# Optimization experiments

Hardware: AMD Instinct MI355X
Metric: run time of the kernel (lower is better)

The kernel has to match this reference:

```python
import jax, jax.numpy as jnp
import numpy as np

B, T, D, H, MLP, NI, OUT = 256, 2049, 64, 64, 128, 128, 10
L = D + D * (D - 1) // 2  # depth-2 logsignature channels = 2080


def _logsig_depth2(X, n_intervals):
    """Depth-2 log-signature of a piecewise-linear path over equal intervals.
    X: [B, T, D] with T = n_intervals*s + 1. Returns [B, n_intervals, L] where
    L = D + D(D-1)/2 (level-1 increments + strictly-upper-triangular Levy areas,
    the Lyndon-word basis signatory uses at depth 2)."""
    Bq, Tq, Dq = X.shape
    s = (Tq - 1) // n_intervals
    idx = np.arange(n_intervals)[:, None] * s + np.arange(s + 1)[None, :]
    seg = X[:, idx]                       # [B, n, s+1, D]
    inc = seg[:, :, -1] - seg[:, :, 0]    # level 1: [B, n, D]
    dlt = seg[:, :, 1:] - seg[:, :, :-1]  # per-step increments [B, n, s, D]
    cum = seg[:, :, :-1] - seg[:, :, :1]  # partial increments  [B, n, s, D]
    M = jnp.einsum('bnki,bnkj->bnij', cum, dlt)
    A = 0.5 * (M - jnp.swapaxes(M, -1, -2))  # Levy area [B, n, D, D]
    iu, ju = np.triu_indices(Dq, 1)
    return jnp.concatenate([inc, A[..., iu, ju]], axis=-1)  # [B, n, L]


def setup_inputs() -> dict:
    key = jax.random.key(0)
    ks = jax.random.split(key, 10)
    X = jax.random.normal(ks[0], (B, T, D), jnp.float32) * 0.05
    W_in = jax.random.normal(ks[1], (D, H), jnp.float32) / np.sqrt(D)
    b_in = jnp.zeros((H,), jnp.float32)
    W1 = jax.random.normal(ks[2], (H, MLP), jnp.float32) / np.sqrt(H)
    b1 = jnp.zeros((MLP,), jnp.float32)
    W2 = jax.random.normal(ks[3], (MLP, D * L), jnp.float32) / np.sqrt(MLP)
    b2 = jnp.zeros((D * L,), jnp.float32)
    W_out = jax.random.normal(ks[4], (H, OUT), jnp.float32) / np.sqrt(H)
    b_out = jnp.zeros((OUT,), jnp.float32)
    return {"X": X, "W_in": W_in, "b_in": b_in, "W1": W1, "b1": b1,
            "W2": W2, "b2": b2, "W_out": W_out, "b_out": b_out,
            "n_intervals": NI}


def reference(X, W_in, b_in, W1, b1, W2, b2, W_out, b_out, n_intervals):
    Bq, Tq, Dq = X.shape
    logsig = _logsig_depth2(X, n_intervals)        # [B, n, L]
    h0 = X[:, 0] @ W_in + b_in                     # initial_linear

    def vf(h):  # F.forward: MLP(h) -> [B, D, L]
        z = jnp.tanh(h @ W1 + b1)
        return (z @ W2 + b2).reshape(Bq, Dq, -1)

    def g(h, ls):  # f(h) contracted with logsig derivative
        return jnp.einsum('bdl,bl->bd', vf(h), ls)

    def rk4_step(h, ls):  # one RK4 step per interval, dt = 1
        k1 = g(h, ls)
        k2 = g(h + 0.5 * k1, ls)
        k3 = g(h + 0.5 * k2, ls)
        k4 = g(h + k3, ls)
        return h + (k1 + 2.0 * k2 + 2.0 * k3 + k4) / 6.0, None

    hT, _ = jax.lax.scan(rk4_step, h0, jnp.swapaxes(logsig, 0, 1))
    return hT @ W_out + b_out  # readout_linear: [B, OUT]
```

## Files before the change

kernel.cpp:

```cpp
#include <hip/hip_runtime.h>
#include <hip/hip_bf16.h>
#include <cstdint>
#include <cstddef>

#define B_SZ   256
#define T_SZ   2049
#define D_SZ   64
#define H_SZ   64
#define MLP_SZ 128
#define NI_SZ  128
#define SEG    16
#define L_SZ   2080
#define NPAIR  2016
#define OUT_SZ 10

#define NC     16
#define NCHUNK (NI_SZ / NC)
#define MROWS  (NC * B_SZ)
#define NCOLS  8320
#define KDIM   L_SZ

typedef _Float16 f16x8 __attribute__((ext_vector_type(8)));
typedef float    f32x4 __attribute__((ext_vector_type(4)));

__device__ __forceinline__ float rlane(float v, int l) {
    return __uint_as_float(__builtin_amdgcn_readlane(__float_as_uint(v), l));
}

__global__ void build_B(const float* __restrict__ W2, const float* __restrict__ b2,
                        _Float16* __restrict__ Bm) {
    const size_t NW = (size_t)8192 * KDIM;
    const size_t NB = NW + (size_t)64 * KDIM;
    const size_t NT = (size_t)NCOLS * KDIM;
    for (size_t i = (size_t)blockIdx.x * blockDim.x + threadIdx.x; i < NT;
         i += (size_t)gridDim.x * blockDim.x) {
        float v = (i < NW) ? W2[i] : ((i < NB) ? b2[i - NW] : 0.0f);
        Bm[i] = (_Float16)v;
    }
}

__global__ void h0_kernel(const float* __restrict__ X, const float* __restrict__ W_in,
                          const float* __restrict__ b_in, float* __restrict__ h_state) {
    const int b = blockIdx.x, t = threadIdx.x;
    __shared__ float x0[D_SZ];
    if (t < D_SZ) x0[t] = X[(size_t)b * T_SZ * D_SZ + t];
    __syncthreads();
    float acc = b_in[t];
    for (int k = 0; k < D_SZ; ++k) acc += x0[k] * W_in[k * H_SZ + t];
    h_state[b * H_SZ + t] = acc;
}

__global__ __launch_bounds__(256) void logsig_kernel(const float* __restrict__ X,
                                                     _Float16* __restrict__ LS,
                                                     int n0) {
    const int b = blockIdx.x, sl = blockIdx.y, t = threadIdx.x;
    const int n = n0 + sl;
    __shared__ float seg[SEG + 1][D_SZ];
    __shared__ float cum[SEG][D_SZ];
    __shared__ float dlt[SEG][D_SZ];
    __shared__ float Mm[D_SZ][D_SZ + 1];

    const float* Xp = X + ((size_t)b * T_SZ + (size_t)n * SEG) * D_SZ;
    for (int i = t; i < (SEG + 1) * D_SZ / 4; i += 256)
        ((float4*)&seg[0][0])[i] = ((const float4*)Xp)[i];
    __syncthreads();
    for (int i = t; i < SEG * D_SZ; i += 256) {
        const int k = i >> 6, d = i & 63;
        cum[k][d] = seg[k][d] - seg[0][d];
        dlt[k][d] = seg[k + 1][d] - seg[k][d];
    }
    __syncthreads();

    const int ti = t >> 4, tj = t & 15;
    const int i0 = ti * 4, j0 = tj * 4;
    float m4[4][4] = {};
#pragma unroll
    for (int k = 0; k < SEG; ++k) {
        const float4 ci = *(const float4*)&cum[k][i0];
        const float4 dj = *(const float4*)&dlt[k][j0];
        const float* cip = (const float*)&ci;
        const float* djp = (const float*)&dj;
#pragma unroll
        for (int a = 0; a < 4; ++a)
#pragma unroll
            for (int c = 0; c < 4; ++c)
                m4[a][c] += cip[a] * djp[c];
    }
#pragma unroll
    for (int a = 0; a < 4; ++a)
#pragma unroll
        for (int c = 0; c < 4; ++c)
            Mm[i0 + a][j0 + c] = m4[a][c];
    __syncthreads();

    _Float16* out = LS + (size_t)(sl * B_SZ + b) * KDIM;
    if (t < D_SZ) out[t] = (_Float16)(seg[SEG][t] - seg[0][t]);
    if (tj >= ti) {
#pragma unroll
        for (int a = 0; a < 4; ++a) {
            const int i = i0 + a;
#pragma unroll
            for (int c = 0; c < 4; ++c) {
                const int j = j0 + c;
                if (j > i) {
                    const int p = 63 * i - (i * (i - 1)) / 2 + (j - i - 1);
                    out[D_SZ + p] = (_Float16)(0.5f * (m4[a][c] - Mm[j][i]));
                }
            }
        }
    }
}

__global__ __launch_bounds__(256) void gemm_bt(const unsigned short* __restrict__ A,
                                               const unsigned short* __restrict__ Bm,
                                               _Float16* __restrict__ C) {
    constexpr int K = KDIM, N = NCOLS;
    __shared__ unsigned short As[128 * 32];
    __shared__ unsigned short Bs[128 * 32];
    const int t = threadIdx.x;
    const int lane = t & 63;
    const int w = t >> 6;
    const int wm = w & 1, wn = w >> 1;
    const int tileM = blockIdx.x * 128;
    const int tileN = blockIdx.y * 128;

    const int c0 = w * 2, c1 = c0 + 1;
    const int rs0 = c0 * 16 + (lane >> 2);
    const int rs1 = c1 * 16 + (lane >> 2);
    const int kc = (lane & 3) * 8;

    const unsigned short* gA0 = A + (size_t)(tileM + rs0) * K + kc;
    const unsigned short* gA1 = A + (size_t)(tileM + rs1) * K + kc;
    const unsigned short* gB0 = Bm + (size_t)(tileN + rs0) * K + kc;
    const unsigned short* gB1 = Bm + (size_t)(tileN + rs1) * K + kc;
    unsigned short* lA0 = As + c0 * 512 + lane * 8;
    unsigned short* lA1 = As + c1 * 512 + lane * 8;
    unsigned short* lB0 = Bs + c0 * 512 + lane * 8;
    unsigned short* lB1 = Bs + c1 * 512 + lane * 8;

    f32x4 acc[4][4] = {};
    const int frow = lane & 15;
    const int fk = (lane >> 4) * 8;

    for (int k0 = 0; k0 < K; k0 += 32) {
        __syncthreads();
        __builtin_amdgcn_global_load_lds((__attribute__((address_space(1))) void*)(gA0 + k0),
                                         (__attribute__((address_space(3))) void*)lA0, 16, 0, 0);
        __builtin_amdgcn_global_load_lds((__attribute__((address_space(1))) void*)(gA1 + k0),
                                         (__attribute__((address_space(3))) void*)lA1, 16, 0, 0);
        __builtin_amdgcn_global_load_lds((__attribute__((address_space(1))) void*)(gB0 + k0),
                                         (__attribute__((address_space(3))) void*)lB0, 16, 0, 0);
        __builtin_amdgcn_global_load_lds((__attribute__((address_space(1))) void*)(gB1 + k0),
                                         (__attribute__((address_space(3))) void*)lB1, 16, 0, 0);
        __syncthreads();

        f16x8 af[4], bfm[4];
#pragma unroll
        for (int mi = 0; mi < 4; ++mi)
            af[mi] = *(const f16x8*)(As + (wm * 64 + mi * 16 + frow) * 32 + fk);
#pragma unroll
        for (int ni = 0; ni < 4; ++ni)
            bfm[ni] = *(const f16x8*)(Bs + (wn * 64 + ni * 16 + frow) * 32 + fk);
#pragma unroll
        for (int mi = 0; mi < 4; ++mi)
#pragma unroll
            for (int ni = 0; ni < 4; ++ni)
                acc[mi][ni] = __builtin_amdgcn_mfma_f32_16x16x32_f16(af[mi], bfm[ni],
                                                                     acc[mi][ni], 0, 0, 0);
    }

    const int erow = (lane >> 4) * 4;
#pragma unroll
    for (int mi = 0; mi < 4; ++mi)
#pragma unroll
        for (int ni = 0; ni < 4; ++ni) {
            const int col = tileN + wn * 64 + ni * 16 + frow;
            const size_t rbase = (size_t)(tileM + wm * 64 + mi * 16 + erow) * N + col;
#pragma unroll
            for (int r = 0; r < 4; ++r)
                C[rbase + (size_t)r * N] = (_Float16)acc[mi][ni][r];
        }
}

__global__ __launch_bounds__(256) void ode_chunk(const _Float16* __restrict__ G,
                                                 const float* __restrict__ W1,
                                                 const float* __restrict__ b1,
                                                 float* __restrict__ h_state) {
    const int b = blockIdx.x, t = threadIdx.x;
    const int lane = t & 63, w = t >> 6;
    const int j0 = w * 32 + (lane & 31);
    __shared__ float ys[D_SZ];
    __shared__ float part[4][D_SZ];

    float w1c[D_SZ];
#pragma unroll
    for (int dd = 0; dd < D_SZ; ++dd) w1c[dd] = W1[dd * MLP_SZ + j0];
    const float b1v = b1[j0];

    float hsv = 0.0f;
    float k_st[4] = {0.f, 0.f, 0.f, 0.f};
    if (w == 0) hsv = h_state[b * H_SZ + lane];

    _Float16 praw[32];
    _Float16 b2pre = (_Float16)0.0f;
    {
        const _Float16* Gr = G + (size_t)b * NCOLS;
#pragma unroll
        for (int q = 0; q < 32; ++q) praw[q] = Gr[(w * 32 + q) * 64 + lane];
        if (w == 0) b2pre = Gr[8192 + lane];
    }

#pragma unroll 1
    for (int s = 0; s < NC; ++s) {
        float gcur[32];
#pragma unroll
        for (int q = 0; q < 32; ++q) gcur[q] = (float)praw[q];
        const float b2cur = (float)b2pre;
        if (s + 1 < NC) {
            const _Float16* Gr = G + (size_t)((s + 1) * B_SZ + b) * NCOLS;
#pragma unroll
            for (int q = 0; q < 32; ++q) praw[q] = Gr[(w * 32 + q) * 64 + lane];
            if (w == 0) b2pre = Gr[8192 + lane];
        }

#pragma unroll
        for (int st = 0; st < 4; ++st) {
            if (w == 0) {
                float y = hsv;
                if (st == 1) y += 0.5f * k_st[0];
                else if (st == 2) y += 0.5f * k_st[1];
                else if (st == 3) y += k_st[2];
                ys[lane] = y;
            }
            __syncthreads();
            float a = 0.0f;
#pragma unroll
            for (int dd = 0; dd < D_SZ; dd += 4) {
                const float4 yv = *(const float4*)&ys[dd];
                a += yv.x * w1c[dd] + yv.y * w1c[dd + 1]
                   + yv.z * w1c[dd + 2] + yv.w * w1c[dd + 3];
            }
            const float x = b1v + a;
            const float ex = __expf(2.0f * x);
            const float z = 1.0f - 2.0f / (ex + 1.0f);
            float a2 = 0.0f;
#pragma unroll
            for (int q = 0; q < 32; ++q)
                a2 += gcur[q] * rlane(z, q);
            part[w][lane] = a2;
            __syncthreads();
            if (w == 0)
                k_st[st] = b2cur + part[0][lane] + part[1][lane]
                         + part[2][lane] + part[3][lane];
        }
        if (w == 0)
            hsv += (k_st[0] + 2.0f * k_st[1] + 2.0f * k_st[2] + k_st[3]) * (1.0f / 6.0f);
    }
    if (w == 0) h_state[b * H_SZ + lane] = hsv;
}

__global__ void out_kernel(const float* __restrict__ h_state, const float* __restrict__ W_out,
                           const float* __restrict__ b_out, float* __restrict__ out) {
    const int b = blockIdx.x, t = threadIdx.x;
    __shared__ float hh[H_SZ];
    hh[t] = h_state[b * H_SZ + t];
    __syncthreads();
    if (t < OUT_SZ) {
        float acc = b_out[t];
        for (int d = 0; d < H_SZ; ++d) acc += hh[d] * W_out[d * OUT_SZ + t];
        out[b * OUT_SZ + t] = acc;
    }
}

extern "C" void kernel_launch(void* const* d_in, const int* in_sizes, int n_in,
                              void* d_out, int out_size, void* d_ws, size_t ws_size,
                              hipStream_t stream) {
    (void)in_sizes; (void)n_in; (void)out_size; (void)ws_size;
    const float* X     = (const float*)d_in[0];
    const float* W_in  = (const float*)d_in[1];
    const float* b_in  = (const float*)d_in[2];
    const float* W1    = (const float*)d_in[3];
    const float* b1    = (const float*)d_in[4];
    const float* W2    = (const float*)d_in[5];
    const float* b2    = (const float*)d_in[6];
    const float* W_out = (const float*)d_in[7];
    const float* b_out = (const float*)d_in[8];
    float* out = (float*)d_out;

    char* ws = (char*)d_ws;
    size_t off = 0;
    auto take = [&](size_t bytes) { void* p = ws + off; off = (off + bytes + 255) & ~(size_t)255; return p; };
    _Float16* Bmat = (_Float16*)take((size_t)NCOLS * KDIM * 2);
    _Float16* LSc  = (_Float16*)take((size_t)MROWS * KDIM * 2);
    _Float16* G    = (_Float16*)take((size_t)MROWS * NCOLS * 2);
    float*    hst  = (float*)take((size_t)B_SZ * H_SZ * 4);

    build_B<<<8192, 256, 0, stream>>>(W2, b2, Bmat);
    h0_kernel<<<B_SZ, H_SZ, 0, stream>>>(X, W_in, b_in, hst);

    for (int c = 0; c < NCHUNK; ++c) {
        logsig_kernel<<<dim3(B_SZ, NC), 256, 0, stream>>>(X, LSc, c * NC);
        gemm_bt<<<dim3(MROWS / 128, NCOLS / 128), 256, 0, stream>>>(
            (const unsigned short*)LSc, (const unsigned short*)Bmat, G);
        ode_chunk<<<B_SZ, 256, 0, stream>>>(G, W1, b1, hst);
    }
    out_kernel<<<B_SZ, H_SZ, 0, stream>>>(hst, W_out, b_out, out);
}
```

Baseline: 2.373 ms.

## Permute G column layout for vectorized loads and drop a barrier per RK4 stage

build_B now writes W2 rows in (d, m) order, so each lane of the ODE kernel reads its 32 G coefficients as four contiguous f16x8 vector loads instead of 32 strided scalar loads. The ODE kernel keeps the hidden state redundantly in every wave and writes a per-wave ys copy. With a double-buffered partial-sum array, each RK4 stage needs one __syncthreads instead of two. The chunk size NC doubles to 32, halving the number of kernel launches per sequence at the cost of a larger G workspace.

```diff
diff --git a/kernel.cpp b/kernel.cpp
--- a/kernel.cpp
+++ b/kernel.cpp
@@ -14,7 +14,7 @@
 #define NPAIR  2016
 #define OUT_SZ 10
 
-#define NC     16
+#define NC     32
 #define NCHUNK (NI_SZ / NC)
 #define MROWS  (NC * B_SZ)
 #define NCOLS  8320
@@ -27,16 +27,20 @@
     return __uint_as_float(__builtin_amdgcn_readlane(__float_as_uint(v), l));
 }
 
-__global__ void build_B(const float* __restrict__ W2, const float* __restrict__ b2,
-                        _Float16* __restrict__ Bm) {
-    const size_t NW = (size_t)8192 * KDIM;
-    const size_t NB = NW + (size_t)64 * KDIM;
-    const size_t NT = (size_t)NCOLS * KDIM;
-    for (size_t i = (size_t)blockIdx.x * blockDim.x + threadIdx.x; i < NT;
-         i += (size_t)gridDim.x * blockDim.x) {
-        float v = (i < NW) ? W2[i] : ((i < NB) ? b2[i - NW] : 0.0f);
-        Bm[i] = (_Float16)v;
-    }
+__global__ __launch_bounds__(256) void build_B(const float* __restrict__ W2,
+                                               const float* __restrict__ b2,
+                                               _Float16* __restrict__ Bm) {
+    const int r = blockIdx.x, t = threadIdx.x;
+    const float* src = nullptr;
+    if (r < 8192) {
+        const int d = r >> 7, m = r & 127;
+        src = W2 + (size_t)m * (64 * KDIM) + (size_t)d * KDIM;
+    } else if (r < 8256) {
+        src = b2 + (size_t)(r - 8192) * KDIM;
+    }
+    _Float16* dst = Bm + (size_t)r * KDIM;
+    for (int l = t; l < KDIM; l += 256)
+        dst[l] = src ? (_Float16)src[l] : (_Float16)0.0f;
 }
 
 __global__ void h0_kernel(const float* __restrict__ X, const float* __restrict__ W_in,
@@ -189,54 +193,50 @@
     const int b = blockIdx.x, t = threadIdx.x;
     const int lane = t & 63, w = t >> 6;
     const int j0 = w * 32 + (lane & 31);
-    __shared__ float ys[D_SZ];
-    __shared__ float part[4][D_SZ];
+    __shared__ float ysw[4][D_SZ];
+    __shared__ float part[2][4][D_SZ];
 
     float w1c[D_SZ];
 #pragma unroll
     for (int dd = 0; dd < D_SZ; ++dd) w1c[dd] = W1[dd * MLP_SZ + j0];
     const float b1v = b1[j0];
 
-    float hsv = 0.0f;
+    float hsv = h_state[b * H_SZ + lane];
+    ysw[w][lane] = hsv;
     float k_st[4] = {0.f, 0.f, 0.f, 0.f};
-    if (w == 0) hsv = h_state[b * H_SZ + lane];
-
-    _Float16 praw[32];
-    _Float16 b2pre = (_Float16)0.0f;
+
+    f16x8 pr[4];
+    _Float16 b2pre;
     {
         const _Float16* Gr = G + (size_t)b * NCOLS;
-#pragma unroll
-        for (int q = 0; q < 32; ++q) praw[q] = Gr[(w * 32 + q) * 64 + lane];
-        if (w == 0) b2pre = Gr[8192 + lane];
+        const f16x8* gp = (const f16x8*)(Gr + lane * 128 + w * 32);
+#pragma unroll
+        for (int v = 0; v < 4; ++v) pr[v] = gp[v];
+        b2pre = Gr[8192 + lane];
     }
 
 #pragma unroll 1
     for (int s = 0; s < NC; ++s) {
         float gcur[32];
 #pragma unroll
-        for (int q = 0; q < 32; ++q) gcur[q] = (float)praw[q];
+        for (int v = 0; v < 4; ++v)
+#pragma unroll
+            for (int e = 0; e < 8; ++e) gcur[v * 8 + e] = (float)pr[v][e];
         const float b2cur = (float)b2pre;
         if (s + 1 < NC) {
             const _Float16* Gr = G + (size_t)((s + 1) * B_SZ + b) * NCOLS;
-#pragma unroll
-            for (int q = 0; q < 32; ++q) praw[q] = Gr[(w * 32 + q) * 64 + lane];
-            if (w == 0) b2pre = Gr[8192 + lane];
+            const f16x8* gp = (const f16x8*)(Gr + lane * 128 + w * 32);
+#pragma unroll
+            for (int v = 0; v < 4; ++v) pr[v] = gp[v];
+            b2pre = Gr[8192 + lane];
         }
 
 #pragma unroll
         for (int st = 0; st < 4; ++st) {
-            if (w == 0) {
-                float y = hsv;
-                if (st == 1) y += 0.5f * k_st[0];
-                else if (st == 2) y += 0.5f * k_st[1];
-                else if (st == 3) y += k_st[2];
-                ys[lane] = y;
-            }
-            __syncthreads();
             float a = 0.0f;
 #pragma unroll
             for (int dd = 0; dd < D_SZ; dd += 4) {
-                const float4 yv = *(const float4*)&ys[dd];
+                const float4 yv = *(const float4*)&ysw[w][dd];
                 a += yv.x * w1c[dd] + yv.y * w1c[dd + 1]
                    + yv.z * w1c[dd + 2] + yv.w * w1c[dd + 3];
             }
@@ -247,14 +247,21 @@
 #pragma unroll
             for (int q = 0; q < 32; ++q)
                 a2 += gcur[q] * rlane(z, q);
-            part[w][lane] = a2;
+            part[st & 1][w][lane] = a2;
             __syncthreads();
-            if (w == 0)
-                k_st[st] = b2cur + part[0][lane] + part[1][lane]
-                         + part[2][lane] + part[3][lane];
+            const float kv = b2cur + part[st & 1][0][lane] + part[st & 1][1][lane]
+                           + part[st & 1][2][lane] + part[st & 1][3][lane];
+            k_st[st] = kv;
+            if (st < 3) {
+                float y = hsv;
+                if (st == 0) y += 0.5f * kv;
+                else if (st == 1) y += 0.5f * kv;
+                else y += kv;
+                ysw[w][lane] = y;
+            }
         }
-        if (w == 0)
-            hsv += (k_st[0] + 2.0f * k_st[1] + 2.0f * k_st[2] + k_st[3]) * (1.0f / 6.0f);
+        hsv += (k_st[0] + 2.0f * k_st[1] + 2.0f * k_st[2] + k_st[3]) * (1.0f / 6.0f);
+        ysw[w][lane] = hsv;
     }
     if (w == 0) h_state[b * H_SZ + lane] = hsv;
 }
@@ -295,7 +302,7 @@
     _Float16* G    = (_Float16*)take((size_t)MROWS * NCOLS * 2);
     float*    hst  = (float*)take((size_t)B_SZ * H_SZ * 4);
 
-    build_B<<<8192, 256, 0, stream>>>(W2, b2, Bmat);
+    build_B<<<NCOLS, 256, 0, stream>>>(W2, b2, Bmat);
     h0_kernel<<<B_SZ, H_SZ, 0, stream>>>(X, W_in, b_in, hst);
 
     for (int c = 0; c < NCHUNK; ++c) {
```

Result: faster. 2.302 ms (-3.0%).
